# Optimization experiments

Hardware: AMD Instinct MI355X
Metric: run time of the kernel (lower is better)

The kernel has to match this reference:

```python
import jax, jax.numpy as jnp
import numpy as np

IN_CHANNELS = 256
NUM_CODES = 32


def setup_inputs() -> dict:
    key = jax.random.key(0)
    k1, k2, k3 = jax.random.split(key, 3)
    std = 1.0 / (NUM_CODES * IN_CHANNELS) ** 0.5
    x = jax.random.normal(k1, (32, IN_CHANNELS, 64, 64), dtype=jnp.float32)
    codewords = jax.random.uniform(k2, (NUM_CODES, IN_CHANNELS), minval=-std, maxval=std, dtype=jnp.float32)
    scale = jax.random.uniform(k3, (NUM_CODES,), minval=-1.0, maxval=0.0, dtype=jnp.float32)
    return {"x": x, "codewords": codewords, "scale": scale}


def _encoding(x, codewords, scale):
    B, C, H, W = x.shape
    # (B, N, C) tokens
    xf = x.reshape(B, C, H * W).transpose(0, 2, 1)
    # scaled L2: scale_k * ||x_bn - c_k||^2, expanded to avoid (B,N,K,C) blowup
    x_sq = jnp.sum(xf * xf, axis=-1, keepdims=True)            # (B, N, 1)
    c_sq = jnp.sum(codewords * codewords, axis=-1)             # (K,)
    xc = jnp.einsum('bnc,kc->bnk', xf, codewords)              # (B, N, K)
    sl2 = scale[None, None, :] * (x_sq - 2.0 * xc + c_sq[None, None, :])
    w = jax.nn.softmax(sl2, axis=2)                            # (B, N, K)
    # aggregate: sum_n w_bnk * (x_bnc - c_kc) = (w^T x) - (sum_n w) * c
    wx = jnp.einsum('bnk,bnc->bkc', w, xf)                     # (B, K, C)
    wsum = jnp.sum(w, axis=1)                                  # (B, K)
    return wx - wsum[:, :, None] * codewords[None, :, :]       # (B, K, C)


def reference(x, codewords, scale):
    return _encoding(x, codewords, scale)
```

## Files before the change

### kernel.cpp

```cpp
#include <hip/hip_runtime.h>


#define CC 256
#define KK 32
#define NN 4096
#define CN (CC*NN)
#define TOK 256
#define CHK 32
#define NCH 8

typedef unsigned int u32;
typedef unsigned short u16;
typedef __fp16 half2_t __attribute__((ext_vector_type(2)));
typedef _Float16 f16x8 __attribute__((ext_vector_type(8)));
typedef float f32x4 __attribute__((ext_vector_type(4)));
typedef u32 u32x2 __attribute__((ext_vector_type(2)));

__device__ __forceinline__ u32 pack2(float a, float b) {
    half2_t h = __builtin_amdgcn_cvt_pkrtz(a, b);
    u32 u;
    __builtin_memcpy(&u, &h, 4);
    return u;
}

__device__ __forceinline__ void bar_lgkm() {
    asm volatile("s_waitcnt lgkmcnt(0)" ::: "memory");
    __builtin_amdgcn_s_barrier();
    __builtin_amdgcn_sched_barrier(0);
}

#define STAGE_LOAD(CT) {                                                     \
    const float* xp = x + (size_t)b * CN + n0 + (CT) * CHK + (l & 7) * 4;    \
    _Pragma("unroll")                                                        \
    for (int it = 0; it < 8; ++it) {                                         \
        int ch = it * 32 + w * 8 + (l >> 3);                                 \
        sf[it] = *(const float4*)(xp + (size_t)ch * NN);                     \
    }                                                                        \
}
#define STAGE_WRITE(XTB, SQB) {                                              \
    float s0 = 0.f, s1 = 0.f, s2 = 0.f, s3 = 0.f;                            \
    int tq = l & 7;                                                          \
    _Pragma("unroll")                                                        \
    for (int it = 0; it < 8; ++it) {                                         \
        int ch = it * 32 + w * 8 + (l >> 3);                                 \
        float4 f = sf[it];                                                   \
        s0 += f.x * f.x; s1 += f.y * f.y;                                    \
        s2 += f.z * f.z; s3 += f.w * f.w;                                    \
        u32 u0 = pack2(f.x, f.y), u1 = pack2(f.z, f.w);                      \
        *(uint2*)(&(XTB)[((ch >> 2) * 2 + (tq >> 2)) * 64 +                  \
                         (ch & 3) * 16 + (tq & 3) * 4]) =                    \
            make_uint2(u0, u1);                                              \
    }                                                                        \
    s0 += __shfl_xor(s0, 8); s0 += __shfl_xor(s0, 16); s0 += __shfl_xor(s0, 32); \
    s1 += __shfl_xor(s1, 8); s1 += __shfl_xor(s1, 16); s1 += __shfl_xor(s1, 32); \
    s2 += __shfl_xor(s2, 8); s2 += __shfl_xor(s2, 16); s2 += __shfl_xor(s2, 32); \
    s3 += __shfl_xor(s3, 8); s3 += __shfl_xor(s3, 16); s3 += __shfl_xor(s3, 32); \
    if (l < 8) *(float4*)&(SQB)[w * 32 + tq * 4] = make_float4(s0, s1, s2, s3);  \
}

__global__ void enc_prep(const float* __restrict__ cw, const float* __restrict__ scale,
                         float* __restrict__ abp4, u16* __restrict__ cwh) {
    int tid = threadIdx.x;
    {
        int k = tid >> 3, p = tid & 7;
        float s = 0.f;
        #pragma unroll
        for (int i = 0; i < 32; ++i) {
            float v = cw[k * 256 + p * 32 + i];
            s += v * v;
        }
        s += __shfl_xor(s, 1);
        s += __shfl_xor(s, 2);
        s += __shfl_xor(s, 4);
        if (p == 0) {
            float A = scale[k];
            abp4[k * 4 + 0] = A;
            abp4[k * 4 + 1] = A * s;
            abp4[k * 4 + 2] = -2.f * A;
            abp4[k * 4 + 3] = 0.f;
        }
    }
    for (int i = 0; i < 32; ++i) {
        int idx = i * 256 + tid;
        union { __fp16 h; u16 u; } cv;
        cv.h = (__fp16)cw[idx];
        cwh[idx] = cv.u;
    }
}

#define PA_ISSUE(KS, P, A0, A1) {                                                \
    asm volatile("ds_read_b64_tr_b16 %0, %1 offset:%2"                           \
                 : "=v"(trA[P][0]) : "v"(A0), "i"((KS) * 2048));                 \
    asm volatile("ds_read_b64_tr_b16 %0, %1 offset:%2"                           \
                 : "=v"(trA[P][1]) : "v"(A0), "i"((KS) * 2048 + 256));           \
    asm volatile("ds_read_b64_tr_b16 %0, %1 offset:%2"                           \
                 : "=v"(trA[P][2]) : "v"(A1), "i"((KS) * 2048));                 \
    asm volatile("ds_read_b64_tr_b16 %0, %1 offset:%2"                           \
                 : "=v"(trA[P][3]) : "v"(A1), "i"((KS) * 2048 + 256));           \
}

__global__ __launch_bounds__(256, 2) void enc_main(
    const float* __restrict__ x, const u16* __restrict__ cwh,
    const float* __restrict__ abp4, u16* __restrict__ wxh, float* __restrict__ wxf,
    float* __restrict__ wsum, int use_partials) {

    __shared__ u16   xt[2][8192];
    __shared__ u16   w2sp[4][1024];
    __shared__ float swsq[2][128];

    const int tid = threadIdx.x;
    const int l   = tid & 63;
    const int w   = tid >> 6;
    const int b   = blockIdx.x >> 4;
    const int blk = blockIdx.x & 15;
    const int n0  = blk * TOK;
    const int lg  = (l >> 4) & 3;

    uint4 cwA[8][2];
    {
        const u32* cwg = (const u32*)cwh + (l & 15) * 128 + lg * 4;
        #pragma unroll
        for (int ks = 0; ks < 8; ++ks) {
            cwA[ks][0] = *(const uint4*)(cwg + ks * 16);
            cwA[ks][1] = *(const uint4*)(cwg + 2048 + ks * 16);
        }
    }
    float Ak[2][4], Bk[2][4], Pk[2][4];
    #pragma unroll
    for (int Mt = 0; Mt < 2; ++Mt)
        #pragma unroll
        for (int r = 0; r < 4; ++r) {
            const float* ap = abp4 + (Mt * 16 + lg * 4 + r) * 4;
            Ak[Mt][r] = ap[0]; Bk[Mt][r] = ap[1]; Pk[Mt][r] = ap[2];
        }

    f32x4 accb[4][2];
    #pragma unroll
    for (int q = 0; q < 4; ++q)
        #pragma unroll
        for (int nk = 0; nk < 2; ++nk)
            accb[q][nk] = (f32x4){0.f, 0.f, 0.f, 0.f};
    float wsacc[2][4];
    #pragma unroll
    for (int Mt = 0; Mt < 2; ++Mt)
        #pragma unroll
        for (int r = 0; r < 4; ++r) wsacc[Mt][r] = 0.f;

    float4 sf[8];

    STAGE_LOAD(0);

    for (int ct = 0; ct < NCH; ++ct) {
        const int p2 = ct & 1;
        u16* xtb = &xt[p2][0];
        float* sqb = &swsq[p2][0];

        STAGE_WRITE(xtb, sqb);
        bar_lgkm();

        if (ct < NCH - 1) STAGE_LOAD(ct + 1);

        const u32 a0 = (u32)(uintptr_t)xtb + (4 * (l >> 4)) * 128 + (l & 15) * 8;
        const u32 a1 = a0 + 128;

        f32x4 acca[2][2];
        #pragma unroll
        for (int Mt = 0; Mt < 2; ++Mt)
            #pragma unroll
            for (int Nt = 0; Nt < 2; ++Nt)
                acca[Mt][Nt] = (f32x4){0.f, 0.f, 0.f, 0.f};
        {
            u32x2 trA[2][4];
            PA_ISSUE(0, 0, a0, a1);
            #pragma unroll
            for (int ks = 0; ks < 8; ++ks) {
                const int p = ks & 1;
                if (ks < 7) {
                    if (p == 0) { PA_ISSUE(ks + 1, 1, a0, a1); }
                    else        { PA_ISSUE(ks + 1, 0, a0, a1); }
                    asm volatile("s_waitcnt lgkmcnt(4)");
                } else {
                    asm volatile("s_waitcnt lgkmcnt(0)");
                }
                __builtin_amdgcn_sched_barrier(0);
                #pragma unroll
                for (int Nt = 0; Nt < 2; ++Nt) {
                    union { uint4 u; f16x8 h; } af;
                    af.u = make_uint4(trA[p][2 * Nt].x, trA[p][2 * Nt].y,
                                      trA[p][2 * Nt + 1].x, trA[p][2 * Nt + 1].y);
                    #pragma unroll
                    for (int Mt = 0; Mt < 2; ++Mt) {
                        union { uint4 u; f16x8 h; } cf;
                        cf.u = cwA[ks][Mt];
                        acca[Mt][Nt] = __builtin_amdgcn_mfma_f32_16x16x32_f16(
                            cf.h, af.h, acca[Mt][Nt], 0, 0, 0);
                    }
                }
            }
        }

        {
            #pragma unroll
            for (int Nt = 0; Nt < 2; ++Nt) {
                int t = Nt * 16 + (l & 15);
                float xq = sqb[t] + sqb[32 + t] + sqb[64 + t] + sqb[96 + t];
                float lgt[2][4];
                float m = -3.4e38f;
                #pragma unroll
                for (int Mt = 0; Mt < 2; ++Mt)
                    #pragma unroll
                    for (int r = 0; r < 4; ++r) {
                        lgt[Mt][r] = fmaf(Ak[Mt][r], xq, Bk[Mt][r]) + Pk[Mt][r] * acca[Mt][Nt][r];
                        m = fmaxf(m, lgt[Mt][r]);
                    }
                m = fmaxf(m, __shfl_xor(m, 16));
                m = fmaxf(m, __shfl_xor(m, 32));
                float s = 0.f, e[2][4];
                #pragma unroll
                for (int Mt = 0; Mt < 2; ++Mt)
                    #pragma unroll
                    for (int r = 0; r < 4; ++r) { e[Mt][r] = __expf(lgt[Mt][r] - m); s += e[Mt][r]; }
                s += __shfl_xor(s, 16);
                s += __shfl_xor(s, 32);
                float rcp = 1.0f / s;
                #pragma unroll
                for (int Mt = 0; Mt < 2; ++Mt)
                    #pragma unroll
                    for (int r = 0; r < 4; ++r) {
                        float wv = e[Mt][r] * rcp;
                        wsacc[Mt][r] += wv;
                        union { __fp16 h; u16 u; } cv;
                        cv.h = (__fp16)wv;
                        w2sp[w][(Mt * 16 + lg * 4 + r) * 32 + Nt * 16 + (l & 15)] = cv.u;
                    }
            }
        }

        {
            f16x8 pB[2];
            #pragma unroll
            for (int nk = 0; nk < 2; ++nk)
                pB[nk] = *(const f16x8*)&w2sp[w][(nk * 16 + (l & 15)) * 32 + lg * 8];
            #pragma unroll
            for (int q = 0; q < 4; ++q) {
                int ch = (w * 4 + q) * 16 + (l & 15);
                const f16x8 xA = *(const f16x8*)&xtb[((ch >> 2) * 2 + (l >> 5)) * 64 +
                                                     (ch & 3) * 16 + ((l >> 4) & 1) * 8];
                #pragma unroll
                for (int nk = 0; nk < 2; ++nk)
                    accb[q][nk] = __builtin_amdgcn_mfma_f32_16x16x32_f16(xA, pB[nk], accb[q][nk], 0, 0, 0);
            }
        }
    }

    #pragma unroll
    for (int Mt = 0; Mt < 2; ++Mt)
        #pragma unroll
        for (int r = 0; r < 4; ++r) {
            float v = wsacc[Mt][r];
            v += __shfl_xor(v, 1); v += __shfl_xor(v, 2);
            v += __shfl_xor(v, 4); v += __shfl_xor(v, 8);
            if (w == 0 && (l & 15) == 0)
                atomicAdd(&wsum[b * KK + Mt * 16 + lg * 4 + r], v);
        }
    if (use_partials) {
        u16* dst = wxh + (size_t)blockIdx.x * 8192;
        #pragma unroll
        for (int q = 0; q < 4; ++q)
            #pragma unroll
            for (int nk = 0; nk < 2; ++nk)
                #pragma unroll
                for (int r = 0; r < 4; ++r) {
                    int ch = (w * 4 + q) * 16 + lg * 4 + r;
                    int k  = nk * 16 + (l & 15);
                    union { __fp16 h; u16 u; } cv;
                    cv.h = (__fp16)accb[q][nk][r];
                    dst[ch * 32 + k] = cv.u;
                }
    } else {
        #pragma unroll
        for (int q = 0; q < 4; ++q)
            #pragma unroll
            for (int nk = 0; nk < 2; ++nk)
                #pragma unroll
                for (int r = 0; r < 4; ++r) {
                    int ch = (w * 4 + q) * 16 + lg * 4 + r;
                    int k  = nk * 16 + (l & 15);
                    atomicAdd(&wxf[(size_t)b * 8192 + k * 256 + ch], accb[q][nk][r]);
                }
    }
}

__global__ void enc_final_part(const u16* __restrict__ wxh, const float* __restrict__ wsum,
                               const float* __restrict__ cw, float* __restrict__ out) {
    int i = blockIdx.x * 256 + threadIdx.x;
    int k = i & 31, c = (i >> 5) & 255, b = i >> 13;
    const u16* p = wxh + (size_t)b * 16 * 8192 + c * 32 + k;
    float s = 0.f;
    #pragma unroll
    for (int j = 0; j < 16; ++j) {
        union { u16 u; __fp16 h; } cv;
        cv.u = p[(size_t)j * 8192];
        s += (float)cv.h;
    }
    out[(size_t)b * 8192 + k * 256 + c] = s - wsum[b * 32 + k] * cw[k * 256 + c];
}
__global__ void enc_final_atomic(const float* __restrict__ wx, const float* __restrict__ wsum,
                                 const float* __restrict__ cw, float* __restrict__ out) {
    int i = blockIdx.x * 256 + threadIdx.x;
    int c = i & 255, k = (i >> 8) & 31, b = i >> 13;
    out[i] = wx[i] - wsum[b * 32 + k] * cw[k * 256 + c];
}

extern "C" void kernel_launch(void* const* d_in, const int* in_sizes, int n_in,
                              void* d_out, int out_size, void* d_ws, size_t ws_size,
                              hipStream_t stream) {
    (void)in_sizes; (void)n_in; (void)out_size;
    const float* x     = (const float*)d_in[0];
    const float* cw    = (const float*)d_in[1];
    const float* scale = (const float*)d_in[2];
    float* out = (float*)d_out;
    float* wsf = (float*)d_ws;

    const size_t need = (size_t)(2097152 + 1024 + 128 + 4096) * 4;
    const int use_partials = (ws_size >= need) ? 1 : 0;

    u16* wxh = (u16*)d_ws;
    float *wxf, *wsum, *abp4;
    u16* cwh;
    if (use_partials) {
        wxf  = wsf;
        wsum = wsf + 2097152;
        abp4 = wsf + 2098176;
        cwh  = (u16*)(wsf + 2098304);
        (void)hipMemsetAsync(wsum, 0, 1024 * sizeof(float), stream);
    } else {
        wxf  = wsf;
        wsum = wsf + 262144;
        abp4 = wsf + 263168;
        cwh  = (u16*)(wsf + 263296);
        (void)hipMemsetAsync(d_ws, 0, 263168 * sizeof(float), stream);
    }

    hipLaunchKernelGGL(enc_prep, dim3(1),   dim3(256), 0, stream, cw, scale, abp4, cwh);
    hipLaunchKernelGGL(enc_main, dim3(512), dim3(256), 0, stream, x, cwh, abp4, wxh, wxf, wsum, use_partials);
    if (use_partials)
        hipLaunchKernelGGL(enc_final_part,   dim3(1024), dim3(256), 0, stream, wxh, wsum, cw, out);
    else
        hipLaunchKernelGGL(enc_final_atomic, dim3(1024), dim3(256), 0, stream, wxf, wsum, cw, out);
}
```

Baseline: 45.25 us.

## Fuse codeword prep into main kernel and replace wsum atomics with partials

```diff
diff --git a/kernel.cpp b/kernel.cpp
--- a/kernel.cpp
+++ b/kernel.cpp
@@ -58,36 +58,6 @@
     if (l < 8) *(float4*)&(SQB)[w * 32 + tq * 4] = make_float4(s0, s1, s2, s3);  \
 }
 
-__global__ void enc_prep(const float* __restrict__ cw, const float* __restrict__ scale,
-                         float* __restrict__ abp4, u16* __restrict__ cwh) {
-    int tid = threadIdx.x;
-    {
-        int k = tid >> 3, p = tid & 7;
-        float s = 0.f;
-        #pragma unroll
-        for (int i = 0; i < 32; ++i) {
-            float v = cw[k * 256 + p * 32 + i];
-            s += v * v;
-        }
-        s += __shfl_xor(s, 1);
-        s += __shfl_xor(s, 2);
-        s += __shfl_xor(s, 4);
-        if (p == 0) {
-            float A = scale[k];
-            abp4[k * 4 + 0] = A;
-            abp4[k * 4 + 1] = A * s;
-            abp4[k * 4 + 2] = -2.f * A;
-            abp4[k * 4 + 3] = 0.f;
-        }
-    }
-    for (int i = 0; i < 32; ++i) {
-        int idx = i * 256 + tid;
-        union { __fp16 h; u16 u; } cv;
-        cv.h = (__fp16)cw[idx];
-        cwh[idx] = cv.u;
-    }
-}
-
 #define PA_ISSUE(KS, P, A0, A1) {                                                \
     asm volatile("ds_read_b64_tr_b16 %0, %1 offset:%2"                           \
                  : "=v"(trA[P][0]) : "v"(A0), "i"((KS) * 2048));                 \
@@ -100,9 +70,9 @@
 }
 
 __global__ __launch_bounds__(256, 2) void enc_main(
-    const float* __restrict__ x, const u16* __restrict__ cwh,
-    const float* __restrict__ abp4, u16* __restrict__ wxh, float* __restrict__ wxf,
-    float* __restrict__ wsum, int use_partials) {
+    const float* __restrict__ x, const float* __restrict__ cw,
+    const float* __restrict__ scale, u16* __restrict__ wxh, float* __restrict__ wxf,
+    float* __restrict__ wsumP, int use_partials) {
 
     __shared__ u16   xt[2][8192];
     __shared__ u16   w2sp[4][1024];
@@ -116,22 +86,36 @@
     const int n0  = blk * TOK;
     const int lg  = (l >> 4) & 3;
 
+    float4 sf[8];
+    STAGE_LOAD(0);
+
     uint4 cwA[8][2];
-    {
-        const u32* cwg = (const u32*)cwh + (l & 15) * 128 + lg * 4;
+    float csqp[2] = {0.f, 0.f};
+    #pragma unroll
+    for (int Mt = 0; Mt < 2; ++Mt) {
+        const float* cwp = cw + (size_t)(Mt * 16 + (l & 15)) * 256 + lg * 8;
         #pragma unroll
         for (int ks = 0; ks < 8; ++ks) {
-            cwA[ks][0] = *(const uint4*)(cwg + ks * 16);
-            cwA[ks][1] = *(const uint4*)(cwg + 2048 + ks * 16);
-        }
+            float4 f0 = *(const float4*)(cwp + ks * 32);
+            float4 f1 = *(const float4*)(cwp + ks * 32 + 4);
+            csqp[Mt] += f0.x * f0.x + f0.y * f0.y + f0.z * f0.z + f0.w * f0.w
+                      + f1.x * f1.x + f1.y * f1.y + f1.z * f1.z + f1.w * f1.w;
+            cwA[ks][Mt] = make_uint4(pack2(f0.x, f0.y), pack2(f0.z, f0.w),
+                                     pack2(f1.x, f1.y), pack2(f1.z, f1.w));
+        }
+        csqp[Mt] += __shfl_xor(csqp[Mt], 16);
+        csqp[Mt] += __shfl_xor(csqp[Mt], 32);
     }
     float Ak[2][4], Bk[2][4], Pk[2][4];
     #pragma unroll
     for (int Mt = 0; Mt < 2; ++Mt)
         #pragma unroll
         for (int r = 0; r < 4; ++r) {
-            const float* ap = abp4 + (Mt * 16 + lg * 4 + r) * 4;
-            Ak[Mt][r] = ap[0]; Bk[Mt][r] = ap[1]; Pk[Mt][r] = ap[2];
+            float A = scale[Mt * 16 + lg * 4 + r];
+            float csqv = __shfl(csqp[Mt], lg * 4 + r);
+            Ak[Mt][r] = A;
+            Bk[Mt][r] = A * csqv;
+            Pk[Mt][r] = -2.f * A;
         }
 
     f32x4 accb[4][2];
@@ -145,10 +129,6 @@
     for (int Mt = 0; Mt < 2; ++Mt)
         #pragma unroll
         for (int r = 0; r < 4; ++r) wsacc[Mt][r] = 0.f;
-
-    float4 sf[8];
-
-    STAGE_LOAD(0);
 
     for (int ct = 0; ct < NCH; ++ct) {
         const int p2 = ct & 1;
@@ -261,7 +241,7 @@
             v += __shfl_xor(v, 1); v += __shfl_xor(v, 2);
             v += __shfl_xor(v, 4); v += __shfl_xor(v, 8);
             if (w == 0 && (l & 15) == 0)
-                atomicAdd(&wsum[b * KK + Mt * 16 + lg * 4 + r], v);
+                wsumP[blockIdx.x * KK + Mt * 16 + lg * 4 + r] = v;
         }
     if (use_partials) {
         u16* dst = wxh + (size_t)blockIdx.x * 8192;
@@ -291,7 +271,7 @@
     }
 }
 
-__global__ void enc_final_part(const u16* __restrict__ wxh, const float* __restrict__ wsum,
+__global__ void enc_final_part(const u16* __restrict__ wxh, const float* __restrict__ wsumP,
                                const float* __restrict__ cw, float* __restrict__ out) {
     int i = blockIdx.x * 256 + threadIdx.x;
     int k = i & 31, c = (i >> 5) & 255, b = i >> 13;
@@ -303,13 +283,22 @@
         cv.u = p[(size_t)j * 8192];
         s += (float)cv.h;
     }
-    out[(size_t)b * 8192 + k * 256 + c] = s - wsum[b * 32 + k] * cw[k * 256 + c];
-}
-__global__ void enc_final_atomic(const float* __restrict__ wx, const float* __restrict__ wsum,
+    float ws = 0.f;
+    #pragma unroll
+    for (int j = 0; j < 16; ++j)
+        ws += wsumP[(b * 16 + j) * 32 + k];
+    out[(size_t)b * 8192 + k * 256 + c] = s - ws * cw[k * 256 + c];
+}
+
+__global__ void enc_final_atomic(const float* __restrict__ wx, const float* __restrict__ wsumP,
                                  const float* __restrict__ cw, float* __restrict__ out) {
     int i = blockIdx.x * 256 + threadIdx.x;
     int c = i & 255, k = (i >> 8) & 31, b = i >> 13;
-    out[i] = wx[i] - wsum[b * 32 + k] * cw[k * 256 + c];
+    float ws = 0.f;
+    #pragma unroll
+    for (int j = 0; j < 16; ++j)
+        ws += wsumP[(b * 16 + j) * 32 + k];
+    out[i] = wx[i] - ws * cw[k * 256 + c];
 }
 
 extern "C" void kernel_launch(void* const* d_in, const int* in_sizes, int n_in,
@@ -322,30 +311,24 @@
     float* out = (float*)d_out;
     float* wsf = (float*)d_ws;
 
-    const size_t need = (size_t)(2097152 + 1024 + 128 + 4096) * 4;
+    const size_t need = (size_t)(2097152 + 16384) * 4;
     const int use_partials = (ws_size >= need) ? 1 : 0;
 
     u16* wxh = (u16*)d_ws;
-    float *wxf, *wsum, *abp4;
-    u16* cwh;
+    float *wxf, *wsumP;
     if (use_partials) {
-        wxf  = wsf;
-        wsum = wsf + 2097152;
-        abp4 = wsf + 2098176;
-        cwh  = (u16*)(wsf + 2098304);
-        (void)hipMemsetAsync(wsum, 0, 1024 * sizeof(float), stream);
+        wxf   = wsf;
+        wsumP = wsf + 2097152;
     } else {
-        wxf  = wsf;
-        wsum = wsf + 262144;
-        abp4 = wsf + 263168;
-        cwh  = (u16*)(wsf + 263296);
-        (void)hipMemsetAsync(d_ws, 0, 263168 * sizeof(float), stream);
-    }
-
-    hipLaunchKernelGGL(enc_prep, dim3(1),   dim3(256), 0, stream, cw, scale, abp4, cwh);
-    hipLaunchKernelGGL(enc_main, dim3(512), dim3(256), 0, stream, x, cwh, abp4, wxh, wxf, wsum, use_partials);
+        wxf   = wsf;
+        wsumP = wsf + 262144;
+        (void)hipMemsetAsync(d_ws, 0, 262144 * sizeof(float), stream);
+    }
+
+    hipLaunchKernelGGL(enc_main, dim3(512), dim3(256), 0, stream,
+                       x, cw, scale, wxh, wxf, wsumP, use_partials);
     if (use_partials)
-        hipLaunchKernelGGL(enc_final_part,   dim3(1024), dim3(256), 0, stream, wxh, wsum, cw, out);
+        hipLaunchKernelGGL(enc_final_part,   dim3(1024), dim3(256), 0, stream, wxh, wsumP, cw, out);
     else
-        hipLaunchKernelGGL(enc_final_atomic, dim3(1024), dim3(256), 0, stream, wxf, wsum, cw, out);
-}
+        hipLaunchKernelGGL(enc_final_atomic, dim3(1024), dim3(256), 0, stream, wxf, wsumP, cw, out);
+}
```

Result: faster. 39.47 us (median of 2 runs) (-12.8%).
